# Kernel tuning notes

Measured on AMD Instinct MI355X. Metric: run time of the kernel, lower is better.

The kernel has to match this reference:

```python
import jax, jax.numpy as jnp
import numpy as np

# ---- Cl(4,1) algebra tables (metric: e1..e4 square to +1, e5 to -1) ----
_METRIC = [1.0, 1.0, 1.0, 1.0, -1.0]

def _popcount(x):
    return bin(x).count('1')

def _gp_blade(a, b):
    # geometric product of basis blades given as bitmasks -> (result_mask, sign)
    s = 1.0
    aa = a >> 1
    swaps = 0
    while aa:
        swaps += _popcount(aa & b)
        aa >>= 1
    if swaps & 1:
        s = -s
    for i in range(5):
        if (a & b) & (1 << i):
            s *= _METRIC[i]
    return a ^ b, s

def _build_gp_map():
    # lane ordering: blades sorted by (grade, bitmask) -> lane 0 scalar, 1..5 vectors, ...
    masks = sorted(range(32), key=lambda m: (_popcount(m), m))
    idx = {m: i for i, m in enumerate(masks)}
    gp = np.zeros((32, 32, 32), dtype=np.float32)
    for a in range(32):
        for b in range(32):
            r, s = _gp_blade(masks[a], masks[b])
            gp[a, b, idx[r]] = s
    return gp

_GP_NP = _build_gp_map()
# signature: scalar part of blade*blade (metric sign per lane)
_SIG_NP = np.array([_GP_NP[k, k, 0] for k in range(32)], dtype=np.float32)

N_HEADS = 8
EPS = 1e-6

def normalize_cl41(x):
    # normalize each 32-lane multivector to unit Euclidean magnitude
    n = jnp.sqrt(jnp.sum(x * x, axis=-1, keepdims=True) + EPS)
    return x / n

def versor_linear(x, w, gp):
    # x: (B,S,I,32), w: (O,I,32), gp: (32,32,32)
    w_op = jnp.einsum('oij,jlk->oilk', w, gp)          # (O,I,32,32)
    out = jnp.einsum('bsil,oilk->bsok', x, w_op)       # (B,S,O,32)
    return normalize_cl41(out)

def setup_inputs() -> dict:
    key = jax.random.key(0)
    ks = jax.random.split(key, 5)
    B, S, D = 2, 2048, 64
    std = 1.0 / (D * 32) ** 0.5
    x = jax.random.normal(ks[0], (B, S, D, 32), dtype=jnp.float32)
    wq = jax.random.normal(ks[1], (D, D, 32), dtype=jnp.float32) * std
    wk = jax.random.normal(ks[2], (D, D, 32), dtype=jnp.float32) * std
    wv = jax.random.normal(ks[3], (D, D, 32), dtype=jnp.float32) * std
    wo = jax.random.normal(ks[4], (D, D, 32), dtype=jnp.float32) * std
    return {'x': x, 'wq': wq, 'wk': wk, 'wv': wv, 'wo': wo}

def reference(x, wq, wk, wv, wo):
    gp = jnp.asarray(_GP_NP)
    sig = jnp.asarray(_SIG_NP)
    B, S, D, _ = x.shape
    H = N_HEADS
    hd = D // H
    def split_heads(t):
        return t.reshape(B, S, H, hd, 32).transpose(0, 2, 1, 3, 4)  # (B,H,S,hd,32)
    q = split_heads(versor_linear(x, wq, gp))
    k = split_heads(versor_linear(x, wk, gp))
    v = split_heads(versor_linear(x, wv, gp))
    q_flat = (q * sig).reshape(B, H, S, hd * 32)
    k_flat = k.reshape(B, H, S, hd * 32)
    score = jnp.einsum('bhqf,bhkf->bhqk', q_flat, k_flat) / (hd ** 0.5)
    attn = jax.nn.softmax(score, axis=-1)
    out = jnp.einsum('bhsi,bhidl->bhsdl', attn, v)      # (B,H,S,hd,32)
    out = out.transpose(0, 2, 1, 3, 4).reshape(B, S, D, 32)
    return versor_linear(out, wo, gp)
```

## Files before the change

### kernel.cpp

```cpp
#include <hip/hip_runtime.h>
#include <hip/hip_bf16.h>


typedef unsigned short u16;
typedef unsigned short u16x8 __attribute__((ext_vector_type(8)));
typedef unsigned short u16x4 __attribute__((ext_vector_type(4)));
typedef short          s16x8 __attribute__((ext_vector_type(8)));
typedef float          f32x4 __attribute__((ext_vector_type(4)));

#define B_DIM 2
#define S_DIM 2048
#define D_DIM 64
#define NH    8
#define HD    256
#define F_DIM 2048
#define TOK   4096

__constant__ int LANE_MASK[32] = {
    0,
    1, 2, 4, 8, 16,
    3, 5, 6, 9, 10, 12, 17, 18, 20, 24,
    7, 11, 13, 14, 19, 21, 22, 25, 26, 28,
    15, 23, 27, 29, 30,
    31};
__constant__ int MASK_LANE[32] = {
    0, 1, 2, 6, 3, 7, 8, 16, 4, 9, 10, 17, 11, 18, 19, 26,
    5, 12, 13, 20, 14, 21, 22, 27, 15, 23, 24, 28, 25, 29, 30, 31};

__device__ __forceinline__ float gp_sign(int a, int b) {
  int swaps = 0;
  int aa = a >> 1;
  while (aa) { swaps += __popc(aa & b); aa >>= 1; }
  float s = (swaps & 1) ? -1.0f : 1.0f;
  if (a & b & 16) s = -s;
  return s;
}

__device__ __forceinline__ u16 f2bf(float f) {
  unsigned u = __float_as_uint(f);
  u += 0x7fffu + ((u >> 16) & 1u);
  return (u16)(u >> 16);
}

__device__ __forceinline__ f32x4 mfma16(s16x8 a, s16x8 b, f32x4 c) {
  return __builtin_amdgcn_mfma_f32_16x16x32_bf16(a, b, c, 0, 0, 0);
}

__device__ __forceinline__ void gload16(const u16* g, u16* l) {
  __builtin_amdgcn_global_load_lds(
      (const __attribute__((address_space(1))) void*)g,
      (__attribute__((address_space(3))) void*)l, 16, 0, 0);
}

__global__ __launch_bounds__(256) void k_cast(const float* __restrict__ x,
                                              u16* __restrict__ xb) {
  int i = blockIdx.x * 256 + threadIdx.x;
  const float4* x4 = (const float4*)x;
  float4 a = x4[2 * i], b = x4[2 * i + 1];
  u16x8 r;
  r[0] = f2bf(a.x); r[1] = f2bf(a.y); r[2] = f2bf(a.z); r[3] = f2bf(a.w);
  r[4] = f2bf(b.x); r[5] = f2bf(b.y); r[6] = f2bf(b.z); r[7] = f2bf(b.w);
  *(u16x8*)&xb[8 * i] = r;
}

__global__ __launch_bounds__(256) void k_buildw(const float* __restrict__ w,
                                                u16* __restrict__ W) {
  __shared__ float wvals[32];
  __shared__ int   jt[1024];
  __shared__ float st[1024];
  const int o = blockIdx.x >> 6, i = blockIdx.x & 63;
  const int tid = threadIdx.x;
  for (int e = tid; e < 1024; e += 256) {
    int k = e >> 5, l = e & 31;
    int mk = LANE_MASK[k], ml = LANE_MASK[l];
    int mj = mk ^ ml;
    jt[e] = MASK_LANE[mj];
    st[e] = gp_sign(mj, ml);
  }
  if (tid < 32) wvals[tid] = w[(o * D_DIM + i) * 32 + tid];
  __syncthreads();
  for (int e = tid; e < 1024; e += 256) {
    int k = e >> 5, l = e & 31;
    size_t off = (size_t)(o * 32 + k) * F_DIM + i * 32 + l;
    W[off] = f2bf(st[e] * wvals[jt[e]]);
  }
}

template <int MODE>
__global__ __launch_bounds__(256) void k_gemm_fused(const u16* __restrict__ A,
                                                    const u16* __restrict__ B,
                                                    u16* __restrict__ outb,
                                                    float* __restrict__ outf) {
  constexpr int K = F_DIM, N = F_DIM;
  __shared__ u16 As[128 * 64];
  __shared__ u16 Bs[128 * 64];
  const int tid = threadIdx.x;
  const int wid = tid >> 6, lane = tid & 63;
  const int row0 = blockIdx.y * 128, col0 = blockIdx.x * 128;
  const int wm = (wid >> 1) * 64, wn = (wid & 1) * 64;
  const int lr = lane & 15, lk = (lane >> 4) * 8;
  const int srow = lane >> 3, scol = (lane & 7) * 8;

  f32x4 acc[4][4];
#pragma unroll
  for (int m = 0; m < 4; ++m)
#pragma unroll
    for (int n = 0; n < 4; ++n) acc[m][n] = (f32x4)0.0f;

  for (int k0 = 0; k0 < K; k0 += 64) {
#pragma unroll
    for (int it = 0; it < 4; ++it) {
      int c = it * 4 + wid;
      gload16(&A[(size_t)(row0 + c * 8 + srow) * K + k0 + scol], &As[c * 512]);
      gload16(&B[(size_t)(col0 + c * 8 + srow) * K + k0 + scol], &Bs[c * 512]);
    }
    __syncthreads();
#pragma unroll
    for (int ks = 0; ks < 64; ks += 32) {
      s16x8 af[4], bf[4];
#pragma unroll
      for (int m = 0; m < 4; ++m)
        af[m] = *(const s16x8*)&As[(wm + m * 16 + lr) * 64 + ks + lk];
#pragma unroll
      for (int n = 0; n < 4; ++n)
        bf[n] = *(const s16x8*)&Bs[(wn + n * 16 + lr) * 64 + ks + lk];
#pragma unroll
      for (int m = 0; m < 4; ++m)
#pragma unroll
        for (int n = 0; n < 4; ++n)
          acc[m][n] = mfma16(af[m], bf[n], acc[m][n]);
    }
    __syncthreads();
  }

  float sc0 = 1.0f, sc1 = 1.0f;
  if (MODE == 1) {
    const float qs = 0.35355339059327373f * 1.4426950408889634f;
    int m0 = LANE_MASK[lr], m1 = LANE_MASK[16 + lr];
    sc0 = gp_sign(m0, m0) * qs;
    sc1 = gp_sign(m1, m1) * qs;
  }
#pragma unroll
  for (int m = 0; m < 4; ++m) {
    int rowb = row0 + wm + m * 16 + (lane >> 4) * 4;
#pragma unroll
    for (int np = 0; np < 2; ++np) {
      int n0 = 2 * np, n1 = n0 + 1;
      int colb = col0 + wn + np * 32 + lr;
      f32x4 inv;
#pragma unroll
      for (int r = 0; r < 4; ++r) {
        float a0 = acc[m][n0][r], a1 = acc[m][n1][r];
        float s2 = a0 * a0 + a1 * a1;
        s2 += __shfl_xor(s2, 1);
        s2 += __shfl_xor(s2, 2);
        s2 += __shfl_xor(s2, 4);
        s2 += __shfl_xor(s2, 8);
        inv[r] = 1.0f / sqrtf(s2 + 1e-6f);
      }
      if (MODE == 3) {
        int bb = rowb >> 11, s0 = rowb & 2047;
        u16x4 p0, p1;
#pragma unroll
        for (int r = 0; r < 4; ++r) {
          p0[r] = f2bf(acc[m][n0][r] * inv[r]);
          p1[r] = f2bf(acc[m][n1][r] * inv[r]);
        }
        *(u16x4*)&outb[((size_t)bb * F_DIM + colb) * S_DIM + s0] = p0;
        *(u16x4*)&outb[((size_t)bb * F_DIM + colb + 16) * S_DIM + s0] = p1;
      } else {
#pragma unroll
        for (int r = 0; r < 4; ++r) {
          size_t o = (size_t)(rowb + r) * N + colb;
          if (MODE == 2) {
            outf[o]      = acc[m][n0][r] * inv[r];
            outf[o + 16] = acc[m][n1][r] * inv[r];
          } else {
            outb[o]      = f2bf(acc[m][n0][r] * inv[r] * sc0);
            outb[o + 16] = f2bf(acc[m][n1][r] * inv[r] * sc1);
          }
        }
      }
    }
  }
}

__global__ __launch_bounds__(256) void k_attn(const u16* __restrict__ qb,
                                              const u16* __restrict__ kb,
                                              const u16* __restrict__ vt,
                                              u16* __restrict__ ao) {
  __shared__ u16 Ks[64][264];
  __shared__ u16 Vts[256][72];
  __shared__ u16 Ps[4][16][72];
  const int tid = threadIdx.x, wid = tid >> 6, lane = tid & 63;
  const int rid = (blockIdx.x & 7) * 64 + (blockIdx.x >> 3);
  const int qblk = rid & 31, bh = rid >> 5;
  const int b = bh >> 3, h = bh & 7;
  const int lr = lane & 15, lk = (lane >> 4) * 8;
  const int q0 = qblk * 64 + wid * 16;

  u16x8 qf[8];
#pragma unroll
  for (int c = 0; c < 8; ++c)
    qf[c] = *(const u16x8*)&qb[(size_t)(b * S_DIM + q0 + lr) * F_DIM +
                               h * HD + c * 32 + lk];

  float mrow[4], lacc[4];
#pragma unroll
  for (int r = 0; r < 4; ++r) { mrow[r] = -1e30f; lacc[r] = 0.0f; }
  f32x4 oacc[16];
#pragma unroll
  for (int d = 0; d < 16; ++d) oacc[d] = (f32x4)0.0f;

  for (int kv0 = 0; kv0 < S_DIM; kv0 += 64) {
#pragma unroll
    for (int i = 0; i < 8; ++i) {
      int c = i * 256 + tid;
      {
        int r = c >> 5, off = (c & 31) * 8;
        *(u16x8*)&Ks[r][off] =
            *(const u16x8*)&kb[(size_t)(b * S_DIM + kv0 + r) * F_DIM + h * HD + off];
      }
      {
        int r = c >> 3, off = (c & 7) * 8;
        *(u16x8*)&Vts[r][off] =
            *(const u16x8*)&vt[((size_t)b * F_DIM + h * HD + r) * S_DIM + kv0 + off];
      }
    }
    __syncthreads();

    f32x4 sacc[4];
#pragma unroll
    for (int n = 0; n < 4; ++n) sacc[n] = (f32x4)0.0f;
#pragma unroll
    for (int c = 0; c < 8; ++c) {
      s16x8 a = *(const s16x8*)&qf[c];
#pragma unroll
      for (int n = 0; n < 4; ++n) {
        s16x8 kf = *(const s16x8*)&Ks[n * 16 + lr][c * 32 + lk];
        sacc[n] = mfma16(a, kf, sacc[n]);
      }
    }

    float pmax[4], need = 0.0f;
#pragma unroll
    for (int r = 0; r < 4; ++r) {
      float mx = fmaxf(fmaxf(sacc[0][r], sacc[1][r]), fmaxf(sacc[2][r], sacc[3][r]));
      mx = fmaxf(mx, __shfl_xor(mx, 1));
      mx = fmaxf(mx, __shfl_xor(mx, 2));
      mx = fmaxf(mx, __shfl_xor(mx, 4));
      mx = fmaxf(mx, __shfl_xor(mx, 8));
      pmax[r] = mx;
      need = fmaxf(need, mx - mrow[r]);
    }
    if (!__all(need <= 8.0f)) {
#pragma unroll
      for (int r = 0; r < 4; ++r) {
        float mnew = fmaxf(mrow[r], pmax[r]);
        float alpha = exp2f(mrow[r] - mnew);
        mrow[r] = mnew;
        lacc[r] *= alpha;
#pragma unroll
        for (int d = 0; d < 16; ++d) oacc[d][r] *= alpha;
      }
    }
#pragma unroll
    for (int n = 0; n < 4; ++n)
#pragma unroll
      for (int r = 0; r < 4; ++r) {
        float p = exp2f(sacc[n][r] - mrow[r]);
        lacc[r] += p;
        Ps[wid][(lane >> 4) * 4 + r][n * 16 + lr] = f2bf(p);
      }

#pragma unroll
    for (int ks = 0; ks < 2; ++ks) {
      s16x8 pf = *(const s16x8*)&Ps[wid][lr][ks * 32 + lk];
#pragma unroll
      for (int d0 = 0; d0 < 16; ++d0) {
        s16x8 vf = *(const s16x8*)&Vts[d0 * 16 + lr][ks * 32 + lk];
        oacc[d0] = mfma16(pf, vf, oacc[d0]);
      }
    }
    __syncthreads();
  }

#pragma unroll
  for (int r = 0; r < 4; ++r) {
    float s = lacc[r];
    s += __shfl_xor(s, 1);
    s += __shfl_xor(s, 2);
    s += __shfl_xor(s, 4);
    s += __shfl_xor(s, 8);
    float inv = 1.0f / s;
    int row = q0 + (lane >> 4) * 4 + r;
#pragma unroll
    for (int d0 = 0; d0 < 16; ++d0)
      ao[(size_t)(b * S_DIM + row) * F_DIM + h * HD + d0 * 16 + lr] =
          f2bf(oacc[d0][r] * inv);
  }
}

extern "C" void kernel_launch(void* const* d_in, const int* in_sizes, int n_in,
                              void* d_out, int out_size, void* d_ws, size_t ws_size,
                              hipStream_t stream) {
  const float* x  = (const float*)d_in[0];
  const float* wq = (const float*)d_in[1];
  const float* wk = (const float*)d_in[2];
  const float* wv = (const float*)d_in[3];
  const float* wo = (const float*)d_in[4];

  char* ws = (char*)d_ws;
  const size_t SZ_XB = (size_t)TOK * F_DIM * sizeof(u16);
  const size_t SZ_W  = (size_t)F_DIM * F_DIM * sizeof(u16);
  u16* Xb = (u16*)(ws);
  u16* Wb = (u16*)(ws + SZ_XB);
  u16* Qb = (u16*)(ws + SZ_XB + SZ_W);
  u16* Kb = Qb + (size_t)TOK * F_DIM;
  u16* Vt = Kb + (size_t)TOK * F_DIM;
  u16* Ao = Xb;

  dim3 gemm_grid(F_DIM / 128, TOK / 128);
  const int bw_blocks = D_DIM * D_DIM;

  k_cast<<<TOK * F_DIM / (256 * 8), 256, 0, stream>>>(x, Xb);

  k_buildw<<<bw_blocks, 256, 0, stream>>>(wq, Wb);
  k_gemm_fused<1><<<gemm_grid, 256, 0, stream>>>(Xb, Wb, Qb, nullptr);

  k_buildw<<<bw_blocks, 256, 0, stream>>>(wk, Wb);
  k_gemm_fused<0><<<gemm_grid, 256, 0, stream>>>(Xb, Wb, Kb, nullptr);

  k_buildw<<<bw_blocks, 256, 0, stream>>>(wv, Wb);
  k_gemm_fused<3><<<gemm_grid, 256, 0, stream>>>(Xb, Wb, Vt, nullptr);

  k_attn<<<B_DIM * NH * (S_DIM / 64), 256, 0, stream>>>(Qb, Kb, Vt, Ao);

  k_buildw<<<bw_blocks, 256, 0, stream>>>(wo, Wb);
  k_gemm_fused<2><<<gemm_grid, 256, 0, stream>>>(Ao, Wb, nullptr, (float*)d_out);
}
```

Baseline: 526.3 us.

## Double-buffer K/V tiles with async loads and 32-row query tiles per wave

Reworks the attention kernel so each wave handles 32 query rows (128 per block), halving the number of blocks and reusing each K/V fragment across two MFMA row tiles. K and V tiles are double-buffered in shared memory using direct global-to-LDS loads (gload16) with XOR swizzling, so the next tile's load overlaps the current tile's compute. The cost is more registers (launch bounds set to one block per SM-equivalent), more shared memory, and fewer blocks (256) to fill the GPU.

```diff
diff --git a/kernel.cpp b/kernel.cpp
--- a/kernel.cpp
+++ b/kernel.cpp
@@ -185,120 +185,164 @@
   }
 }
 
-__global__ __launch_bounds__(256) void k_attn(const u16* __restrict__ qb,
-                                              const u16* __restrict__ kb,
-                                              const u16* __restrict__ vt,
-                                              u16* __restrict__ ao) {
-  __shared__ u16 Ks[64][264];
-  __shared__ u16 Vts[256][72];
-  __shared__ u16 Ps[4][16][72];
+__global__ __launch_bounds__(256, 1) void k_attn(const u16* __restrict__ qb,
+                                                 const u16* __restrict__ kb,
+                                                 const u16* __restrict__ vt,
+                                                 u16* __restrict__ ao) {
+  __shared__ u16 Kbuf[2][64 * 256];
+  __shared__ u16 Vbuf[2][256 * 64];
+  __shared__ u16 Ps[4][32][72];
   const int tid = threadIdx.x, wid = tid >> 6, lane = tid & 63;
-  const int rid = (blockIdx.x & 7) * 64 + (blockIdx.x >> 3);
-  const int qblk = rid & 31, bh = rid >> 5;
+  const int rid = (blockIdx.x & 7) * 32 + (blockIdx.x >> 3);
+  const int qblk = rid & 15, bh = rid >> 4;
   const int b = bh >> 3, h = bh & 7;
-  const int lr = lane & 15, lk = (lane >> 4) * 8;
-  const int q0 = qblk * 64 + wid * 16;
-
-  u16x8 qf[8];
-#pragma unroll
-  for (int c = 0; c < 8; ++c)
-    qf[c] = *(const u16x8*)&qb[(size_t)(b * S_DIM + q0 + lr) * F_DIM +
-                               h * HD + c * 32 + lk];
-
-  float mrow[4], lacc[4];
-#pragma unroll
-  for (int r = 0; r < 4; ++r) { mrow[r] = -1e30f; lacc[r] = 0.0f; }
-  f32x4 oacc[16];
-#pragma unroll
-  for (int d = 0; d < 16; ++d) oacc[d] = (f32x4)0.0f;
-
-  for (int kv0 = 0; kv0 < S_DIM; kv0 += 64) {
-#pragma unroll
-    for (int i = 0; i < 8; ++i) {
-      int c = i * 256 + tid;
-      {
-        int r = c >> 5, off = (c & 31) * 8;
-        *(u16x8*)&Ks[r][off] =
-            *(const u16x8*)&kb[(size_t)(b * S_DIM + kv0 + r) * F_DIM + h * HD + off];
-      }
-      {
-        int r = c >> 3, off = (c & 7) * 8;
-        *(u16x8*)&Vts[r][off] =
-            *(const u16x8*)&vt[((size_t)b * F_DIM + h * HD + r) * S_DIM + kv0 + off];
+  const int lr = lane & 15, hi = lane >> 4;
+  const int lr7s = (lr & 7) << 3;
+  const int q0 = qblk * 128 + wid * 32;
+
+  const int krow_l = lane >> 5;
+  const int kcolb  = (lane & 31) * 8;
+  const int vrow_l = lane >> 3;
+  const int vcol_l = ((lane & 7) * 8) ^ ((vrow_l & 7) << 3);
+
+  u16x8 qf[2][8];
+#pragma unroll
+  for (int m = 0; m < 2; ++m)
+#pragma unroll
+    for (int c = 0; c < 8; ++c)
+      qf[m][c] = *(const u16x8*)&qb[(size_t)(b * S_DIM + q0 + m * 16 + lr) * F_DIM +
+                                    h * HD + c * 32 + hi * 8];
+
+  float mrow[2][4], lacc[2][4];
+#pragma unroll
+  for (int m = 0; m < 2; ++m)
+#pragma unroll
+    for (int r = 0; r < 4; ++r) { mrow[m][r] = -1e30f; lacc[m][r] = 0.0f; }
+  f32x4 oacc[2][16];
+#pragma unroll
+  for (int m = 0; m < 2; ++m)
+#pragma unroll
+    for (int d = 0; d < 16; ++d) oacc[m][d] = (f32x4)0.0f;
+
+  const u16* kbase = kb + (size_t)b * S_DIM * F_DIM + h * HD;
+  const u16* vbase = vt + ((size_t)b * F_DIM + h * HD) * S_DIM;
+
+#pragma unroll
+  for (int i = 0; i < 8; ++i) {
+    int ck = wid * 8 + i;
+    int kr = ck * 2 + krow_l;
+    gload16(kbase + (size_t)kr * F_DIM + (kcolb ^ ((kr & 7) << 3)),
+            &Kbuf[0][ck * 512]);
+    int vr = ck * 8 + vrow_l;
+    gload16(vbase + (size_t)vr * S_DIM + vcol_l, &Vbuf[0][ck * 512]);
+  }
+  __syncthreads();
+
+  for (int t = 0; t < 32; ++t) {
+    const int cur = t & 1;
+    if (t < 31) {
+      int kv1 = (t + 1) * 64;
+#pragma unroll
+      for (int i = 0; i < 8; ++i) {
+        int ck = wid * 8 + i;
+        int kr = ck * 2 + krow_l;
+        gload16(kbase + (size_t)(kv1 + kr) * F_DIM + (kcolb ^ ((kr & 7) << 3)),
+                &Kbuf[cur ^ 1][ck * 512]);
+        int vr = ck * 8 + vrow_l;
+        gload16(vbase + (size_t)vr * S_DIM + kv1 + vcol_l,
+                &Vbuf[cur ^ 1][ck * 512]);
+      }
+    }
+
+    f32x4 sacc[2][4];
+#pragma unroll
+    for (int m = 0; m < 2; ++m)
+#pragma unroll
+      for (int n = 0; n < 4; ++n) sacc[m][n] = (f32x4)0.0f;
+#pragma unroll
+    for (int c = 0; c < 8; ++c) {
+      s16x8 kf[4];
+#pragma unroll
+      for (int n = 0; n < 4; ++n)
+        kf[n] = *(const s16x8*)&Kbuf[cur][(n * 16 + lr) * 256 +
+                                          ((c * 32 + hi * 8) ^ lr7s)];
+#pragma unroll
+      for (int m = 0; m < 2; ++m) {
+        s16x8 a = *(const s16x8*)&qf[m][c];
+#pragma unroll
+        for (int n = 0; n < 4; ++n) sacc[m][n] = mfma16(a, kf[n], sacc[m][n]);
+      }
+    }
+
+    float pmax[2][4], need = 0.0f;
+#pragma unroll
+    for (int m = 0; m < 2; ++m)
+#pragma unroll
+      for (int r = 0; r < 4; ++r) {
+        float mx = fmaxf(fmaxf(sacc[m][0][r], sacc[m][1][r]),
+                         fmaxf(sacc[m][2][r], sacc[m][3][r]));
+        mx = fmaxf(mx, __shfl_xor(mx, 1));
+        mx = fmaxf(mx, __shfl_xor(mx, 2));
+        mx = fmaxf(mx, __shfl_xor(mx, 4));
+        mx = fmaxf(mx, __shfl_xor(mx, 8));
+        pmax[m][r] = mx;
+        need = fmaxf(need, mx - mrow[m][r]);
+      }
+    if (!__all(need <= 8.0f)) {
+#pragma unroll
+      for (int m = 0; m < 2; ++m)
+#pragma unroll
+        for (int r = 0; r < 4; ++r) {
+          float mnew = fmaxf(mrow[m][r], pmax[m][r]);
+          float alpha = exp2f(mrow[m][r] - mnew);
+          mrow[m][r] = mnew;
+          lacc[m][r] *= alpha;
+#pragma unroll
+          for (int d = 0; d < 16; ++d) oacc[m][d][r] *= alpha;
+        }
+    }
+#pragma unroll
+    for (int m = 0; m < 2; ++m)
+#pragma unroll
+      for (int n = 0; n < 4; ++n)
+#pragma unroll
+        for (int r = 0; r < 4; ++r) {
+          float p = exp2f(sacc[m][n][r] - mrow[m][r]);
+          lacc[m][r] += p;
+          Ps[wid][m * 16 + hi * 4 + r][n * 16 + lr] = f2bf(p);
+        }
+
+#pragma unroll
+    for (int ks = 0; ks < 2; ++ks) {
+      s16x8 pf0 = *(const s16x8*)&Ps[wid][lr][ks * 32 + hi * 8];
+      s16x8 pf1 = *(const s16x8*)&Ps[wid][16 + lr][ks * 32 + hi * 8];
+#pragma unroll
+      for (int d0 = 0; d0 < 16; ++d0) {
+        s16x8 vf = *(const s16x8*)&Vbuf[cur][(d0 * 16 + lr) * 64 +
+                                             ((ks * 32 + hi * 8) ^ lr7s)];
+        oacc[0][d0] = mfma16(pf0, vf, oacc[0][d0]);
+        oacc[1][d0] = mfma16(pf1, vf, oacc[1][d0]);
       }
     }
     __syncthreads();
-
-    f32x4 sacc[4];
-#pragma unroll
-    for (int n = 0; n < 4; ++n) sacc[n] = (f32x4)0.0f;
-#pragma unroll
-    for (int c = 0; c < 8; ++c) {
-      s16x8 a = *(const s16x8*)&qf[c];
-#pragma unroll
-      for (int n = 0; n < 4; ++n) {
-        s16x8 kf = *(const s16x8*)&Ks[n * 16 + lr][c * 32 + lk];
-        sacc[n] = mfma16(a, kf, sacc[n]);
-      }
-    }
-
-    float pmax[4], need = 0.0f;
+  }
+
+#pragma unroll
+  for (int m = 0; m < 2; ++m)
 #pragma unroll
     for (int r = 0; r < 4; ++r) {
-      float mx = fmaxf(fmaxf(sacc[0][r], sacc[1][r]), fmaxf(sacc[2][r], sacc[3][r]));
-      mx = fmaxf(mx, __shfl_xor(mx, 1));
-      mx = fmaxf(mx, __shfl_xor(mx, 2));
-      mx = fmaxf(mx, __shfl_xor(mx, 4));
-      mx = fmaxf(mx, __shfl_xor(mx, 8));
-      pmax[r] = mx;
-      need = fmaxf(need, mx - mrow[r]);
-    }
-    if (!__all(need <= 8.0f)) {
-#pragma unroll
-      for (int r = 0; r < 4; ++r) {
-        float mnew = fmaxf(mrow[r], pmax[r]);
-        float alpha = exp2f(mrow[r] - mnew);
-        mrow[r] = mnew;
-        lacc[r] *= alpha;
-#pragma unroll
-        for (int d = 0; d < 16; ++d) oacc[d][r] *= alpha;
-      }
-    }
-#pragma unroll
-    for (int n = 0; n < 4; ++n)
-#pragma unroll
-      for (int r = 0; r < 4; ++r) {
-        float p = exp2f(sacc[n][r] - mrow[r]);
-        lacc[r] += p;
-        Ps[wid][(lane >> 4) * 4 + r][n * 16 + lr] = f2bf(p);
-      }
-
-#pragma unroll
-    for (int ks = 0; ks < 2; ++ks) {
-      s16x8 pf = *(const s16x8*)&Ps[wid][lr][ks * 32 + lk];
-#pragma unroll
-      for (int d0 = 0; d0 < 16; ++d0) {
-        s16x8 vf = *(const s16x8*)&Vts[d0 * 16 + lr][ks * 32 + lk];
-        oacc[d0] = mfma16(pf, vf, oacc[d0]);
-      }
-    }
-    __syncthreads();
-  }
-
-#pragma unroll
-  for (int r = 0; r < 4; ++r) {
-    float s = lacc[r];
-    s += __shfl_xor(s, 1);
-    s += __shfl_xor(s, 2);
-    s += __shfl_xor(s, 4);
-    s += __shfl_xor(s, 8);
-    float inv = 1.0f / s;
-    int row = q0 + (lane >> 4) * 4 + r;
-#pragma unroll
-    for (int d0 = 0; d0 < 16; ++d0)
-      ao[(size_t)(b * S_DIM + row) * F_DIM + h * HD + d0 * 16 + lr] =
-          f2bf(oacc[d0][r] * inv);
-  }
+      float s = lacc[m][r];
+      s += __shfl_xor(s, 1);
+      s += __shfl_xor(s, 2);
+      s += __shfl_xor(s, 4);
+      s += __shfl_xor(s, 8);
+      float inv = 1.0f / s;
+      int row = q0 + m * 16 + hi * 4 + r;
+#pragma unroll
+      for (int d0 = 0; d0 < 16; ++d0)
+        ao[(size_t)(b * S_DIM + row) * F_DIM + h * HD + d0 * 16 + lr] =
+            f2bf(oacc[m][d0][r] * inv);
+    }
 }
 
 extern "C" void kernel_launch(void* const* d_in, const int* in_sizes, int n_in,
@@ -334,7 +378,7 @@
   k_buildw<<<bw_blocks, 256, 0, stream>>>(wv, Wb);
   k_gemm_fused<3><<<gemm_grid, 256, 0, stream>>>(Xb, Wb, Vt, nullptr);
 
-  k_attn<<<B_DIM * NH * (S_DIM / 64), 256, 0, stream>>>(Qb, Kb, Vt, Ao);
+  k_attn<<<B_DIM * NH * (S_DIM / 128), 256, 0, stream>>>(Qb, Kb, Vt, Ao);
 
   k_buildw<<<bw_blocks, 256, 0, stream>>>(wo, Wb);
   k_gemm_fused<2><<<gemm_grid, 256, 0, stream>>>(Ao, Wb, nullptr, (float*)d_out);
```

Measured after the change: 538.5 us. +2.3%, slower.

## Double-buffer K/V tiles with direct LDS loads and swizzled layout in attention

Applied to the files above, without the earlier changes.

The attention kernel now uses 512-thread blocks covering 128 queries, so each K/V tile is shared by twice as many query rows. The next K and V tiles are loaded into a second shared-memory buffer with direct global-to-LDS loads while the current tile is computed. Row padding is replaced by an XOR swizzle to avoid bank conflicts. The cost is about 146KB of LDS per block, which allows at most one block per CU despite the launch bound, and correctness relies on the async loads being complete before the barrier.

```diff
diff --git a/kernel.cpp b/kernel.cpp
--- a/kernel.cpp
+++ b/kernel.cpp
@@ -185,25 +185,31 @@
   }
 }
 
-__global__ __launch_bounds__(256) void k_attn(const u16* __restrict__ qb,
-                                              const u16* __restrict__ kb,
-                                              const u16* __restrict__ vt,
-                                              u16* __restrict__ ao) {
-  __shared__ u16 Ks[64][264];
-  __shared__ u16 Vts[256][72];
-  __shared__ u16 Ps[4][16][72];
+__global__ __launch_bounds__(512, 2) void k_attn(const u16* __restrict__ qb,
+                                                 const u16* __restrict__ kb,
+                                                 const u16* __restrict__ vt,
+                                                 u16* __restrict__ ao) {
+  __shared__ u16 Kbuf[2][64 * 256];
+  __shared__ u16 Vbuf[2][256 * 64];
+  __shared__ u16 Ps[8][16][72];
   const int tid = threadIdx.x, wid = tid >> 6, lane = tid & 63;
-  const int rid = (blockIdx.x & 7) * 64 + (blockIdx.x >> 3);
-  const int qblk = rid & 31, bh = rid >> 5;
+  const int rid = (blockIdx.x & 7) * 32 + (blockIdx.x >> 3);
+  const int qblk = rid & 15, bh = rid >> 4;
   const int b = bh >> 3, h = bh & 7;
-  const int lr = lane & 15, lk = (lane >> 4) * 8;
-  const int q0 = qblk * 64 + wid * 16;
+  const int lr = lane & 15, hi = lane >> 4;
+  const int lr7s = (lr & 7) << 3;
+  const int q0 = qblk * 128 + wid * 16;
+
+  const int krow_l = lane >> 5;
+  const int kcolb  = (lane & 31) * 8;
+  const int vrow_l = lane >> 3;
+  const int vcol_l = ((lane & 7) * 8) ^ ((vrow_l & 7) << 3);
 
   u16x8 qf[8];
 #pragma unroll
   for (int c = 0; c < 8; ++c)
     qf[c] = *(const u16x8*)&qb[(size_t)(b * S_DIM + q0 + lr) * F_DIM +
-                               h * HD + c * 32 + lk];
+                               h * HD + c * 32 + hi * 8];
 
   float mrow[4], lacc[4];
 #pragma unroll
@@ -212,22 +218,35 @@
 #pragma unroll
   for (int d = 0; d < 16; ++d) oacc[d] = (f32x4)0.0f;
 
-  for (int kv0 = 0; kv0 < S_DIM; kv0 += 64) {
-#pragma unroll
-    for (int i = 0; i < 8; ++i) {
-      int c = i * 256 + tid;
-      {
-        int r = c >> 5, off = (c & 31) * 8;
-        *(u16x8*)&Ks[r][off] =
-            *(const u16x8*)&kb[(size_t)(b * S_DIM + kv0 + r) * F_DIM + h * HD + off];
-      }
-      {
-        int r = c >> 3, off = (c & 7) * 8;
-        *(u16x8*)&Vts[r][off] =
-            *(const u16x8*)&vt[((size_t)b * F_DIM + h * HD + r) * S_DIM + kv0 + off];
-      }
-    }
-    __syncthreads();
+  const u16* kbase = kb + (size_t)b * S_DIM * F_DIM + h * HD;
+  const u16* vbase = vt + ((size_t)b * F_DIM + h * HD) * S_DIM;
+
+#pragma unroll
+  for (int i = 0; i < 4; ++i) {
+    int ck = wid * 4 + i;
+    int kr = ck * 2 + krow_l;
+    gload16(kbase + (size_t)kr * F_DIM + (kcolb ^ ((kr & 7) << 3)),
+            &Kbuf[0][ck * 512]);
+    int vr = ck * 8 + vrow_l;
+    gload16(vbase + (size_t)vr * S_DIM + vcol_l, &Vbuf[0][ck * 512]);
+  }
+  __syncthreads();
+
+  for (int t = 0; t < 32; ++t) {
+    const int cur = t & 1;
+    if (t < 31) {
+      int kv1 = (t + 1) * 64;
+#pragma unroll
+      for (int i = 0; i < 4; ++i) {
+        int ck = wid * 4 + i;
+        int kr = ck * 2 + krow_l;
+        gload16(kbase + (size_t)(kv1 + kr) * F_DIM + (kcolb ^ ((kr & 7) << 3)),
+                &Kbuf[cur ^ 1][ck * 512]);
+        int vr = ck * 8 + vrow_l;
+        gload16(vbase + (size_t)vr * S_DIM + kv1 + vcol_l,
+                &Vbuf[cur ^ 1][ck * 512]);
+      }
+    }
 
     f32x4 sacc[4];
 #pragma unroll
@@ -237,7 +256,8 @@
       s16x8 a = *(const s16x8*)&qf[c];
 #pragma unroll
       for (int n = 0; n < 4; ++n) {
-        s16x8 kf = *(const s16x8*)&Ks[n * 16 + lr][c * 32 + lk];
+        s16x8 kf = *(const s16x8*)&Kbuf[cur][(n * 16 + lr) * 256 +
+                                             ((c * 32 + hi * 8) ^ lr7s)];
         sacc[n] = mfma16(a, kf, sacc[n]);
       }
     }
@@ -245,7 +265,8 @@
     float pmax[4], need = 0.0f;
 #pragma unroll
     for (int r = 0; r < 4; ++r) {
-      float mx = fmaxf(fmaxf(sacc[0][r], sacc[1][r]), fmaxf(sacc[2][r], sacc[3][r]));
+      float mx = fmaxf(fmaxf(sacc[0][r], sacc[1][r]),
+                       fmaxf(sacc[2][r], sacc[3][r]));
       mx = fmaxf(mx, __shfl_xor(mx, 1));
       mx = fmaxf(mx, __shfl_xor(mx, 2));
       mx = fmaxf(mx, __shfl_xor(mx, 4));
@@ -270,15 +291,16 @@
       for (int r = 0; r < 4; ++r) {
         float p = exp2f(sacc[n][r] - mrow[r]);
         lacc[r] += p;
-        Ps[wid][(lane >> 4) * 4 + r][n * 16 + lr] = f2bf(p);
+        Ps[wid][hi * 4 + r][n * 16 + lr] = f2bf(p);
       }
 
 #pragma unroll
     for (int ks = 0; ks < 2; ++ks) {
-      s16x8 pf = *(const s16x8*)&Ps[wid][lr][ks * 32 + lk];
+      s16x8 pf = *(const s16x8*)&Ps[wid][lr][ks * 32 + hi * 8];
 #pragma unroll
       for (int d0 = 0; d0 < 16; ++d0) {
-        s16x8 vf = *(const s16x8*)&Vts[d0 * 16 + lr][ks * 32 + lk];
+        s16x8 vf = *(const s16x8*)&Vbuf[cur][(d0 * 16 + lr) * 64 +
+                                             ((ks * 32 + hi * 8) ^ lr7s)];
         oacc[d0] = mfma16(pf, vf, oacc[d0]);
       }
     }
@@ -293,7 +315,7 @@
     s += __shfl_xor(s, 4);
     s += __shfl_xor(s, 8);
     float inv = 1.0f / s;
-    int row = q0 + (lane >> 4) * 4 + r;
+    int row = q0 + hi * 4 + r;
 #pragma unroll
     for (int d0 = 0; d0 < 16; ++d0)
       ao[(size_t)(b * S_DIM + row) * F_DIM + h * HD + d0 * 16 + lr] =
@@ -334,7 +356,7 @@
   k_buildw<<<bw_blocks, 256, 0, stream>>>(wv, Wb);
   k_gemm_fused<3><<<gemm_grid, 256, 0, stream>>>(Xb, Wb, Vt, nullptr);
 
-  k_attn<<<B_DIM * NH * (S_DIM / 64), 256, 0, stream>>>(Qb, Kb, Vt, Ao);
+  k_attn<<<B_DIM * NH * (S_DIM / 128), 512, 0, stream>>>(Qb, Kb, Vt, Ao);
 
   k_buildw<<<bw_blocks, 256, 0, stream>>>(wo, Wb);
   k_gemm_fused<2><<<gemm_grid, 256, 0, stream>>>(Ao, Wb, nullptr, (float*)d_out);
```

Result: faster. 444.0 us (-15.6%).
